# Kernel optimization log

Hardware: AMD Instinct MI355X
Metric: run time of the kernel (lower is better)

Reference implementation:

```python
import jax, jax.numpy as jnp
import numpy as np

G = 4      # deformable groups
K = 9      # 3x3 kernel points
EPS = 1e-5


def _bilinear_gather(value, loc_y, loc_x):
    # value: (N,H,W,G,Cg); loc_*: (N,H,W,G,K) float pixel coords, zero padding outside.
    N, H, W, g, Cg = value.shape
    y0f = jnp.floor(loc_y); x0f = jnp.floor(loc_x)
    wy = loc_y - y0f; wx = loc_x - x0f
    y0 = y0f.astype(jnp.int32); x0 = x0f.astype(jnp.int32)
    n_idx = jnp.arange(N).reshape(N, 1, 1, 1, 1)
    g_idx = jnp.arange(g).reshape(1, 1, 1, g, 1)

    def corner(yi, xi, w):
        valid = (yi >= 0) & (yi < H) & (xi >= 0) & (xi < W)
        yc = jnp.clip(yi, 0, H - 1); xc = jnp.clip(xi, 0, W - 1)
        v = value[n_idx, yc, xc, g_idx]  # (N,H,W,G,K,Cg) irregular gather
        return v * (w * valid)[..., None]

    return (corner(y0, x0, (1 - wy) * (1 - wx))
            + corner(y0, x0 + 1, (1 - wy) * wx)
            + corner(y0 + 1, x0, wy * (1 - wx))
            + corner(y0 + 1, x0 + 1, wy * wx))


def _dcnv4(t, H, W, Wv, bv, Wom, bom, Wo):
    # DCNv4 on (N,L,C): value proj -> learned-offset bilinear sampling with
    # UNNORMALIZED dynamic weights (no softmax, DCNv4) -> output proj (no bias).
    N, L, C = t.shape
    Cg = C // G
    value = (t @ Wv + bv).reshape(N, H, W, G, Cg)
    om = (t @ Wom + bom).reshape(N, H, W, G, 3 * K)
    offset = om[..., :2 * K].reshape(N, H, W, G, K, 2)  # (dx, dy) per point
    mask = om[..., 2 * K:]                               # (N,H,W,G,K)
    ky, kx = jnp.meshgrid(jnp.arange(-1, 2), jnp.arange(-1, 2), indexing='ij')
    ky = ky.reshape(-1).astype(t.dtype); kx = kx.reshape(-1).astype(t.dtype)
    ys = jnp.arange(H, dtype=t.dtype).reshape(1, H, 1, 1, 1)
    xs = jnp.arange(W, dtype=t.dtype).reshape(1, 1, W, 1, 1)
    loc_y = ys + ky + offset[..., 1]  # (N,H,W,G,K)
    loc_x = xs + kx + offset[..., 0]
    sampled = _bilinear_gather(value, loc_y, loc_x)  # (N,H,W,G,K,Cg)
    out = (sampled * mask[..., None]).sum(axis=4)    # (N,H,W,G,Cg)
    return out.reshape(N, L, C) @ Wo


def _bn(x, gamma, beta):
    # training-mode BatchNorm2d: per-channel batch stats over (N,H,W)
    mean = x.mean(axis=(0, 2, 3), keepdims=True)
    var = ((x - mean) ** 2).mean(axis=(0, 2, 3), keepdims=True)
    return (x - mean) * jax.lax.rsqrt(var + EPS) * gamma.reshape(1, -1, 1, 1) \
        + beta.reshape(1, -1, 1, 1)


def setup_inputs() -> dict:
    key = jax.random.key(0)
    ks = jax.random.split(key, 6)
    N, C, H, W = 4, 128, 64, 64
    s = 1.0 / np.sqrt(C)
    x = jax.random.normal(ks[0], (N, C, H, W), jnp.float32)
    Wv = jax.random.normal(ks[1], (C, C), jnp.float32) * s      # value_proj
    bv = jnp.zeros((C,), jnp.float32)
    Wom = jax.random.normal(ks[2], (C, G * 3 * K), jnp.float32) * 0.01  # offset+mask head
    bom = jnp.zeros((G * 3 * K,), jnp.float32)
    Wo = jax.random.normal(ks[3], (C, C), jnp.float32) * s      # output_proj (bias=False)
    gamma = jnp.ones((C,), jnp.float32)
    beta = jnp.zeros((C,), jnp.float32)
    Wc = jax.random.normal(ks[4], (C, C), jnp.float32) * s      # 1x1 conv (out=in=C)
    return {"x": x, "Wv": Wv, "bv": bv, "Wom": Wom, "bom": bom,
            "Wo": Wo, "gamma": gamma, "beta": beta, "Wc": Wc}


def reference(x, Wv, bv, Wom, bom, Wo, gamma, beta, Wc):
    N, C, H, W = x.shape
    shortcut = x
    t = x.transpose(0, 2, 3, 1).reshape(N, H * W, C)
    t = _dcnv4(t, H, W, Wv, bv, Wom, bom, Wo)
    y = t.reshape(N, H, W, C).transpose(0, 3, 1, 2)
    y = jax.nn.relu(_bn(y, gamma, beta))
    t = y.transpose(0, 2, 3, 1).reshape(N, H * W, C)
    t = _dcnv4(t, H, W, Wv, bv, Wom, bom, Wo)  # same DCNv4 weights reused
    y = t.reshape(N, H, W, C).transpose(0, 3, 1, 2)
    y = _bn(y, gamma, beta)                    # same BN params reused, no relu here
    y = y + shortcut                           # in_channels == out_channels
    return jnp.einsum('nchw,oc->nohw', y, Wc)  # final 1x1 conv
```

## Files before the change

### kernel.cpp

```cpp
#include <hip/hip_runtime.h>
#include <math.h>

#define CC   128
#define NL   16384
#define LHW  4096
#define OMP  112
#define HH   64
#define WW   64

typedef __attribute__((ext_vector_type(8))) short short8;
typedef __attribute__((ext_vector_type(4))) float f32x4;

__device__ __forceinline__ unsigned short f2bf(float f) {
    union { float f; unsigned u; } v; v.f = f;
    unsigned r = v.u + 0x7fff + ((v.u >> 16) & 1);
    return (unsigned short)(r >> 16);
}
__device__ __forceinline__ float bf2f(unsigned short u) {
    union { unsigned u; float f; } v; v.u = ((unsigned)u) << 16;
    return v.f;
}

__global__ __launch_bounds__(256) void prep_kernel(
    const float* __restrict__ Wv, const float* __restrict__ Wom,
    const float* __restrict__ Wo, const float* __restrict__ Wc,
    unsigned short* __restrict__ Wcomb, unsigned short* __restrict__ WoT,
    unsigned short* __restrict__ Wcb, float* __restrict__ stats)
{
    int tid = threadIdx.x;
    if (blockIdx.x == 0) {
        stats[tid] = 0.0f;
        stats[256 + tid] = 0.0f;
    }
    int i = blockIdx.x * 256 + tid;
    if (i < 16384) {
        int n = i >> 7, k = i & 127;
        Wcomb[i] = f2bf(Wv[k * CC + n]);
    } else if (i < 30720) {
        int j = i - 16384; int n = j >> 7, k = j & 127;
        Wcomb[16384 + j] = (n < 108) ? f2bf(Wom[k * 108 + n]) : (unsigned short)0;
    } else if (i < 47104) {
        int j = i - 30720; int n = j >> 7, k = j & 127;
        WoT[j] = f2bf(Wo[k * CC + n]);
    } else if (i < 63488) {
        int j = i - 47104;
        Wcb[j] = f2bf(Wc[j]);
    }
}

template<int IN_MODE>
__global__ __launch_bounds__(256) void gemm_vom_kernel(
    const float* __restrict__ Ain, const unsigned short* __restrict__ Wcomb,
    const float* __restrict__ bv, const float* __restrict__ bom,
    const float* __restrict__ stats, const float* __restrict__ gamma,
    const float* __restrict__ beta,
    unsigned short* __restrict__ val, float* __restrict__ omb)
{
    __shared__ unsigned short As[64 * 136];
    __shared__ unsigned short Bs[240 * 136];
    __shared__ float bnsc[128], bnsh[128];

    int tid = threadIdx.x;
    int block_m = blockIdx.x * 64;

    if (IN_MODE == 1 && tid < 128) {
        const float inv = 1.0f / 16384.0f;
        float mean = stats[tid] * inv;
        float var  = stats[128 + tid] * inv - mean * mean;
        float sc   = rsqrtf(var + 1e-5f) * gamma[tid];
        bnsc[tid] = sc;
        bnsh[tid] = beta[tid] - mean * sc;
    }

#pragma unroll
    for (int i = 0; i < 15; i++) {
        int id = tid + i * 256;
        int r = id >> 4, kc = id & 15;
        float4 v = *(const float4*)(Wcomb + (size_t)r * CC + kc * 8);
        *(float4*)(&Bs[r * 136 + kc * 8]) = v;
    }

    if (IN_MODE == 0) {
        int n   = block_m >> 12;
        int hw0 = block_m & 4095;
#pragma unroll
        for (int i = 0; i < 8; i++) {
            int id = tid + i * 256;
            int c  = id >> 4, j4 = id & 15;
            float4 v = *(const float4*)(Ain + (((size_t)(n * CC + c)) << 12) + hw0 + j4 * 4);
            As[(j4 * 4 + 0) * 136 + c] = f2bf(v.x);
            As[(j4 * 4 + 1) * 136 + c] = f2bf(v.y);
            As[(j4 * 4 + 2) * 136 + c] = f2bf(v.z);
            As[(j4 * 4 + 3) * 136 + c] = f2bf(v.w);
        }
    } else {
        __syncthreads();
#pragma unroll
        for (int i = 0; i < 8; i++) {
            int id = tid + i * 256;
            int r  = id >> 5, c4 = id & 31;
            float4 v = *(const float4*)(Ain + (size_t)(block_m + r) * CC + c4 * 4);
            int c = c4 * 4;
            float a0 = fmaxf(v.x * bnsc[c + 0] + bnsh[c + 0], 0.0f);
            float a1 = fmaxf(v.y * bnsc[c + 1] + bnsh[c + 1], 0.0f);
            float a2 = fmaxf(v.z * bnsc[c + 2] + bnsh[c + 2], 0.0f);
            float a3 = fmaxf(v.w * bnsc[c + 3] + bnsh[c + 3], 0.0f);
            As[r * 136 + c + 0] = f2bf(a0);
            As[r * 136 + c + 1] = f2bf(a1);
            As[r * 136 + c + 2] = f2bf(a2);
            As[r * 136 + c + 3] = f2bf(a3);
        }
    }
    __syncthreads();

    int w  = tid >> 6;
    int l  = tid & 63;
    int lr = l & 15, lk = l >> 4;

    f32x4 acc[15];
#pragma unroll
    for (int nt = 0; nt < 15; nt++) acc[nt] = (f32x4){0.f, 0.f, 0.f, 0.f};

#pragma unroll
    for (int kk = 0; kk < 4; kk++) {
        short8 a = *(const short8*)(&As[(w * 16 + lr) * 136 + kk * 32 + lk * 8]);
#pragma unroll
        for (int nt = 0; nt < 15; nt++) {
            short8 b = *(const short8*)(&Bs[(nt * 16 + lr) * 136 + kk * 32 + lk * 8]);
            acc[nt] = __builtin_amdgcn_mfma_f32_16x16x32_bf16(a, b, acc[nt], 0, 0, 0);
        }
    }

    int row0 = block_m + w * 16 + lk * 4;
#pragma unroll
    for (int nt = 0; nt < 8; nt++) {
        int col = nt * 16 + lr;
        float bb = bv[col];
#pragma unroll
        for (int r = 0; r < 4; r++)
            val[(size_t)(row0 + r) * CC + col] = f2bf(acc[nt][r] + bb);
    }
#pragma unroll
    for (int nt = 8; nt < 15; nt++) {
        int col = (nt - 8) * 16 + lr;
        float bb = (col < 108) ? bom[col] : 0.0f;
#pragma unroll
        for (int r = 0; r < 4; r++)
            omb[(size_t)(row0 + r) * OMP + col] = acc[nt][r] + bb;
    }
}

__global__ __launch_bounds__(256) void sample_kernel(
    const unsigned short* __restrict__ val, const float* __restrict__ omb,
    unsigned int* __restrict__ sbuf)
{
    int tid    = threadIdx.x;
    int gid    = blockIdx.x * 256 + tid;
    int unit   = gid >> 4;
    int lane16 = gid & 15;
    int nl = unit >> 2;
    int g  = unit & 3;
    int n  = nl >> 12;
    int hw = nl & 4095;
    int h  = hw >> 6;
    int w  = hw & 63;

    const float* omp = omb + (size_t)nl * OMP + g * 27;
    const unsigned short* vb = val + (((size_t)n) << 19) + g * 32 + lane16 * 2;

    float acc0 = 0.0f, acc1 = 0.0f;
#pragma unroll
    for (int k = 0; k < 9; k++) {
        float ox = omp[2 * k];
        float oy = omp[2 * k + 1];
        float mk = omp[18 + k];
        float ly = (float)(h + k / 3 - 1) + oy;
        float lx = (float)(w + k % 3 - 1) + ox;
        float y0f = floorf(ly), x0f = floorf(lx);
        float wy = ly - y0f, wx = lx - x0f;
        int y0 = (int)y0f, x0 = (int)x0f;

        float v0 = 0.0f, v1 = 0.0f;
#pragma unroll
        for (int cy = 0; cy < 2; cy++) {
#pragma unroll
            for (int cx = 0; cx < 2; cx++) {
                int yi = y0 + cy, xi = x0 + cx;
                float wgt = (cy ? wy : 1.0f - wy) * (cx ? wx : 1.0f - wx);
                bool valid = (yi >= 0) && (yi < HH) && (xi >= 0) && (xi < WW);
                wgt = valid ? wgt : 0.0f;
                int yc = min(max(yi, 0), HH - 1);
                int xc = min(max(xi, 0), WW - 1);
                unsigned int pv = *(const unsigned int*)(vb + (size_t)(yc * WW + xc) * CC);
                v0 += bf2f((unsigned short)(pv & 0xffff)) * wgt;
                v1 += bf2f((unsigned short)(pv >> 16)) * wgt;
            }
        }
        acc0 += mk * v0;
        acc1 += mk * v1;
    }
    unsigned int packed = (unsigned int)f2bf(acc0) | ((unsigned int)f2bf(acc1) << 16);
    sbuf[(size_t)nl * 64 + g * 16 + lane16] = packed;
}

__global__ __launch_bounds__(256) void gemm_o_bn_kernel(
    const unsigned short* __restrict__ A, const unsigned short* __restrict__ Bt,
    float* __restrict__ ybuf, float* __restrict__ stats)
{
    __shared__ unsigned short As[64 * 136];
    __shared__ unsigned short Bs[128 * 136];
    __shared__ float lstat[256];

    int tid = threadIdx.x;
    int block_m = blockIdx.x * 64;
    lstat[tid] = 0.0f;

#pragma unroll
    for (int i = 0; i < 4; i++) {
        int id = tid + i * 256;
        int r = id >> 4, kc = id & 15;
        float4 v = *(const float4*)(A + (size_t)(block_m + r) * CC + kc * 8);
        *(float4*)(&As[r * 136 + kc * 8]) = v;
    }
#pragma unroll
    for (int i = 0; i < 8; i++) {
        int id = tid + i * 256;
        int r = id >> 4, kc = id & 15;
        float4 v = *(const float4*)(Bt + (size_t)r * CC + kc * 8);
        *(float4*)(&Bs[r * 136 + kc * 8]) = v;
    }
    __syncthreads();

    int w  = tid >> 6;
    int l  = tid & 63;
    int wm = w & 1, wn = w >> 1;
    int lr = l & 15, lk = l >> 4;

    f32x4 acc[2][4];
#pragma unroll
    for (int mt = 0; mt < 2; mt++)
#pragma unroll
        for (int nt = 0; nt < 4; nt++) acc[mt][nt] = (f32x4){0.f, 0.f, 0.f, 0.f};

#pragma unroll
    for (int kk = 0; kk < 4; kk++) {
        short8 a[2], b[4];
#pragma unroll
        for (int mt = 0; mt < 2; mt++)
            a[mt] = *(const short8*)(&As[(wm * 32 + mt * 16 + lr) * 136 + kk * 32 + lk * 8]);
#pragma unroll
        for (int nt = 0; nt < 4; nt++)
            b[nt] = *(const short8*)(&Bs[(wn * 64 + nt * 16 + lr) * 136 + kk * 32 + lk * 8]);
#pragma unroll
        for (int mt = 0; mt < 2; mt++)
#pragma unroll
            for (int nt = 0; nt < 4; nt++)
                acc[mt][nt] = __builtin_amdgcn_mfma_f32_16x16x32_bf16(
                    a[mt], b[nt], acc[mt][nt], 0, 0, 0);
    }

#pragma unroll
    for (int nt = 0; nt < 4; nt++) {
        int col = wn * 64 + nt * 16 + lr;
        float s = 0.0f, sq = 0.0f;
#pragma unroll
        for (int mt = 0; mt < 2; mt++) {
            int row0 = block_m + wm * 32 + mt * 16 + lk * 4;
#pragma unroll
            for (int r = 0; r < 4; r++) {
                float v = acc[mt][nt][r];
                ybuf[(size_t)(row0 + r) * CC + col] = v;
                s += v;
                sq += v * v;
            }
        }
        atomicAdd(&lstat[col], s);
        atomicAdd(&lstat[128 + col], sq);
    }
    __syncthreads();
    if (tid < 128) {
        atomicAdd(&stats[tid], lstat[tid]);
        atomicAdd(&stats[128 + tid], lstat[128 + tid]);
    }
}

__global__ __launch_bounds__(256) void gemm_final_kernel(
    const float* __restrict__ ybuf, const float* __restrict__ x,
    const unsigned short* __restrict__ Bt, const float* __restrict__ stats,
    const float* __restrict__ gamma, const float* __restrict__ beta,
    float* __restrict__ out)
{
    __shared__ unsigned short As[64 * 136];
    __shared__ unsigned short Bs[128 * 136];
    __shared__ float Xs[64 * 132];
    __shared__ float bnsc[128], bnsh[128];

    int tid = threadIdx.x;
    int block_m = blockIdx.x * 64;
    int n   = block_m >> 12;
    int hw0 = block_m & 4095;

    if (tid < 128) {
        const float inv = 1.0f / 16384.0f;
        float mean = stats[tid] * inv;
        float var  = stats[128 + tid] * inv - mean * mean;
        float sc   = rsqrtf(var + 1e-5f) * gamma[tid];
        bnsc[tid] = sc;
        bnsh[tid] = beta[tid] - mean * sc;
    }

#pragma unroll
    for (int i = 0; i < 8; i++) {
        int id = tid + i * 256;
        int c  = id >> 4, j4 = id & 15;
        float4 v = *(const float4*)(x + (((size_t)(n * CC + c)) << 12) + hw0 + j4 * 4);
        Xs[(j4 * 4 + 0) * 132 + c] = v.x;
        Xs[(j4 * 4 + 1) * 132 + c] = v.y;
        Xs[(j4 * 4 + 2) * 132 + c] = v.z;
        Xs[(j4 * 4 + 3) * 132 + c] = v.w;
    }
#pragma unroll
    for (int i = 0; i < 8; i++) {
        int id = tid + i * 256;
        int r = id >> 4, kc = id & 15;
        float4 v = *(const float4*)(Bt + (size_t)r * CC + kc * 8);
        *(float4*)(&Bs[r * 136 + kc * 8]) = v;
    }
    __syncthreads();

#pragma unroll
    for (int i = 0; i < 8; i++) {
        int id = tid + i * 256;
        int r  = id >> 5, c4 = id & 31;
        float4 v = *(const float4*)(ybuf + (size_t)(block_m + r) * CC + c4 * 4);
        int c = c4 * 4;
        float a0 = v.x * bnsc[c + 0] + bnsh[c + 0] + Xs[r * 132 + c + 0];
        float a1 = v.y * bnsc[c + 1] + bnsh[c + 1] + Xs[r * 132 + c + 1];
        float a2 = v.z * bnsc[c + 2] + bnsh[c + 2] + Xs[r * 132 + c + 2];
        float a3 = v.w * bnsc[c + 3] + bnsh[c + 3] + Xs[r * 132 + c + 3];
        As[r * 136 + c + 0] = f2bf(a0);
        As[r * 136 + c + 1] = f2bf(a1);
        As[r * 136 + c + 2] = f2bf(a2);
        As[r * 136 + c + 3] = f2bf(a3);
    }
    __syncthreads();

    int w  = tid >> 6;
    int l  = tid & 63;
    int wm = w & 1, wn = w >> 1;
    int lr = l & 15, lk = l >> 4;

    f32x4 acc[2][4];
#pragma unroll
    for (int mt = 0; mt < 2; mt++)
#pragma unroll
        for (int nt = 0; nt < 4; nt++) acc[mt][nt] = (f32x4){0.f, 0.f, 0.f, 0.f};

#pragma unroll
    for (int kk = 0; kk < 4; kk++) {
        short8 a[2], b[4];
#pragma unroll
        for (int mt = 0; mt < 2; mt++)
            a[mt] = *(const short8*)(&As[(wm * 32 + mt * 16 + lr) * 136 + kk * 32 + lk * 8]);
#pragma unroll
        for (int nt = 0; nt < 4; nt++)
            b[nt] = *(const short8*)(&Bs[(wn * 64 + nt * 16 + lr) * 136 + kk * 32 + lk * 8]);
#pragma unroll
        for (int mt = 0; mt < 2; mt++)
#pragma unroll
            for (int nt = 0; nt < 4; nt++)
                acc[mt][nt] = __builtin_amdgcn_mfma_f32_16x16x32_bf16(
                    a[mt], b[nt], acc[mt][nt], 0, 0, 0);
    }

    __syncthreads();
    float* T = (float*)Bs;
#pragma unroll
    for (int mt = 0; mt < 2; mt++) {
        int rloc = wm * 32 + mt * 16 + lk * 4;
#pragma unroll
        for (int nt = 0; nt < 4; nt++) {
            int col = wn * 64 + nt * 16 + lr;
#pragma unroll
            for (int r = 0; r < 4; r++)
                T[col * 68 + rloc + r] = acc[mt][nt][r];
        }
    }
    __syncthreads();
    int o = tid >> 1, half = tid & 1;
    float* op = out + (((size_t)(n * CC + o)) << 12) + hw0 + half * 32;
#pragma unroll
    for (int i = 0; i < 8; i++) {
        float4 v = *(const float4*)(&T[o * 68 + half * 32 + i * 4]);
        *(float4*)(op + i * 4) = v;
    }
}

extern "C" void kernel_launch(void* const* d_in, const int* in_sizes, int n_in,
                              void* d_out, int out_size, void* d_ws, size_t ws_size,
                              hipStream_t stream)
{
    const float* x     = (const float*)d_in[0];
    const float* Wv    = (const float*)d_in[1];
    const float* bv    = (const float*)d_in[2];
    const float* Wom   = (const float*)d_in[3];
    const float* bom   = (const float*)d_in[4];
    const float* Wo    = (const float*)d_in[5];
    const float* gamma = (const float*)d_in[6];
    const float* beta  = (const float*)d_in[7];
    const float* Wc    = (const float*)d_in[8];
    float* out = (float*)d_out;

    char* ws = (char*)d_ws;
    unsigned short* val   = (unsigned short*)ws;   ws += (size_t)NL * CC * 2;
    float*          omb   = (float*)ws;            ws += (size_t)NL * OMP * 4;
    unsigned int*   sbuf  = (unsigned int*)ws;     ws += (size_t)NL * CC * 2;
    float*          ybuf  = (float*)ws;            ws += (size_t)NL * CC * 4;
    unsigned short* Wcomb = (unsigned short*)ws;   ws += 240 * 128 * 2;
    unsigned short* WoT   = (unsigned short*)ws;   ws += 128 * 128 * 2;
    unsigned short* Wcb   = (unsigned short*)ws;   ws += 128 * 128 * 2;
    float*          stats = (float*)ws;            ws += 2048;

    dim3 b256(256);

    prep_kernel<<<248, b256, 0, stream>>>(Wv, Wom, Wo, Wc, Wcomb, WoT, Wcb, stats);

    gemm_vom_kernel<0><<<256, b256, 0, stream>>>(x, Wcomb, bv, bom,
                                                 nullptr, nullptr, nullptr, val, omb);
    sample_kernel<<<4096, b256, 0, stream>>>(val, omb, sbuf);
    gemm_o_bn_kernel<<<256, b256, 0, stream>>>((const unsigned short*)sbuf, WoT, ybuf, stats);

    gemm_vom_kernel<1><<<256, b256, 0, stream>>>(ybuf, Wcomb, bv, bom,
                                                 stats, gamma, beta, val, omb);
    sample_kernel<<<4096, b256, 0, stream>>>(val, omb, sbuf);
    gemm_o_bn_kernel<<<256, b256, 0, stream>>>((const unsigned short*)sbuf, WoT, ybuf, stats + 256);

    gemm_final_kernel<<<256, b256, 0, stream>>>(ybuf, x, Wcb, stats + 256, gamma, beta, out);
}
```

Baseline: 157.5 us.

## Shrink GEMM tiles to 16 rows, read weights from global, shard BN stats atomics

All GEMM kernels now process 16-row tiles with 1024 blocks instead of 64-row tiles with 256 blocks. The B weight tiles are no longer staged in shared memory; MFMA operands are loaded straight from global memory, which relies on L2/L1 caching of the small bf16 weight matrices. BN statistics are accumulated into 8 sharded slots that consumers sum, to reduce atomic contention on one address set. The aim is higher occupancy and better CU coverage on the small GEMMs, at the cost of redundant global weight reads and uncoalesced fragment loads.

```diff
diff --git a/kernel.cpp b/kernel.cpp
--- a/kernel.cpp
+++ b/kernel.cpp
@@ -3,7 +3,6 @@
 
 #define CC   128
 #define NL   16384
-#define LHW  4096
 #define OMP  112
 #define HH   64
 #define WW   64
@@ -28,22 +27,21 @@
     unsigned short* __restrict__ Wcb, float* __restrict__ stats)
 {
     int tid = threadIdx.x;
-    if (blockIdx.x == 0) {
-        stats[tid] = 0.0f;
-        stats[256 + tid] = 0.0f;
-    }
-    int i = blockIdx.x * 256 + tid;
-    if (i < 16384) {
-        int n = i >> 7, k = i & 127;
-        Wcomb[i] = f2bf(Wv[k * CC + n]);
-    } else if (i < 30720) {
-        int j = i - 16384; int n = j >> 7, k = j & 127;
-        Wcomb[16384 + j] = (n < 108) ? f2bf(Wom[k * 108 + n]) : (unsigned short)0;
-    } else if (i < 47104) {
-        int j = i - 30720; int n = j >> 7, k = j & 127;
-        WoT[j] = f2bf(Wo[k * CC + n]);
-    } else if (i < 63488) {
-        int j = i - 47104;
+    int b   = blockIdx.x;
+    if (b < 16) stats[b * 256 + tid] = 0.0f;
+    int i = b * 256 + tid;
+    if (i < 32768) {
+        int r = i >> 7, k = i & 127;
+        unsigned short v;
+        if (r < 128)      v = f2bf(Wv[k * CC + r]);
+        else if (r < 240) { int nn = r - 128; v = (nn < 108) ? f2bf(Wom[k * 108 + nn]) : (unsigned short)0; }
+        else              v = 0;
+        Wcomb[i] = v;
+    } else if (i < 49152) {
+        int j = i - 32768; int nn = j >> 7, k = j & 127;
+        WoT[j] = f2bf(Wo[k * CC + nn]);
+    } else {
+        int j = i - 49152;
         Wcb[j] = f2bf(Wc[j]);
     }
 }
@@ -56,37 +54,37 @@
     const float* __restrict__ beta,
     unsigned short* __restrict__ val, float* __restrict__ omb)
 {
-    __shared__ unsigned short As[64 * 136];
-    __shared__ unsigned short Bs[240 * 136];
+    __shared__ unsigned short As[16 * 136];
     __shared__ float bnsc[128], bnsh[128];
 
     int tid = threadIdx.x;
-    int block_m = blockIdx.x * 64;
-
-    if (IN_MODE == 1 && tid < 128) {
-        const float inv = 1.0f / 16384.0f;
-        float mean = stats[tid] * inv;
-        float var  = stats[128 + tid] * inv - mean * mean;
-        float sc   = rsqrtf(var + 1e-5f) * gamma[tid];
-        bnsc[tid] = sc;
-        bnsh[tid] = beta[tid] - mean * sc;
-    }
-
-#pragma unroll
-    for (int i = 0; i < 15; i++) {
-        int id = tid + i * 256;
-        int r = id >> 4, kc = id & 15;
-        float4 v = *(const float4*)(Wcomb + (size_t)r * CC + kc * 8);
-        *(float4*)(&Bs[r * 136 + kc * 8]) = v;
+    int block_m = blockIdx.x * 16;
+
+    if (IN_MODE == 1) {
+        if (tid < 128) {
+            float s = 0.0f, sq = 0.0f;
+#pragma unroll
+            for (int g = 0; g < 8; g++) {
+                s  += stats[g * 256 + tid];
+                sq += stats[g * 256 + 128 + tid];
+            }
+            const float inv = 1.0f / 16384.0f;
+            float mean = s * inv;
+            float var  = sq * inv - mean * mean;
+            float sc   = rsqrtf(var + 1e-5f) * gamma[tid];
+            bnsc[tid] = sc;
+            bnsh[tid] = beta[tid] - mean * sc;
+        }
+        __syncthreads();
     }
 
     if (IN_MODE == 0) {
         int n   = block_m >> 12;
         int hw0 = block_m & 4095;
 #pragma unroll
-        for (int i = 0; i < 8; i++) {
+        for (int i = 0; i < 2; i++) {
             int id = tid + i * 256;
-            int c  = id >> 4, j4 = id & 15;
+            int c  = id >> 2, j4 = id & 3;
             float4 v = *(const float4*)(Ain + (((size_t)(n * CC + c)) << 12) + hw0 + j4 * 4);
             As[(j4 * 4 + 0) * 136 + c] = f2bf(v.x);
             As[(j4 * 4 + 1) * 136 + c] = f2bf(v.y);
@@ -94,21 +92,15 @@
             As[(j4 * 4 + 3) * 136 + c] = f2bf(v.w);
         }
     } else {
-        __syncthreads();
-#pragma unroll
-        for (int i = 0; i < 8; i++) {
+#pragma unroll
+        for (int i = 0; i < 2; i++) {
             int id = tid + i * 256;
-            int r  = id >> 5, c4 = id & 31;
-            float4 v = *(const float4*)(Ain + (size_t)(block_m + r) * CC + c4 * 4);
-            int c = c4 * 4;
-            float a0 = fmaxf(v.x * bnsc[c + 0] + bnsh[c + 0], 0.0f);
-            float a1 = fmaxf(v.y * bnsc[c + 1] + bnsh[c + 1], 0.0f);
-            float a2 = fmaxf(v.z * bnsc[c + 2] + bnsh[c + 2], 0.0f);
-            float a3 = fmaxf(v.w * bnsc[c + 3] + bnsh[c + 3], 0.0f);
-            As[r * 136 + c + 0] = f2bf(a0);
-            As[r * 136 + c + 1] = f2bf(a1);
-            As[r * 136 + c + 2] = f2bf(a2);
-            As[r * 136 + c + 3] = f2bf(a3);
+            int r  = id >> 5, c = (id & 31) * 4;
+            float4 v = *(const float4*)(Ain + (size_t)(block_m + r) * CC + c);
+            As[r * 136 + c + 0] = f2bf(fmaxf(v.x * bnsc[c + 0] + bnsh[c + 0], 0.0f));
+            As[r * 136 + c + 1] = f2bf(fmaxf(v.y * bnsc[c + 1] + bnsh[c + 1], 0.0f));
+            As[r * 136 + c + 2] = f2bf(fmaxf(v.z * bnsc[c + 2] + bnsh[c + 2], 0.0f));
+            As[r * 136 + c + 3] = f2bf(fmaxf(v.w * bnsc[c + 3] + bnsh[c + 3], 0.0f));
         }
     }
     __syncthreads();
@@ -117,36 +109,37 @@
     int l  = tid & 63;
     int lr = l & 15, lk = l >> 4;
 
-    f32x4 acc[15];
-#pragma unroll
-    for (int nt = 0; nt < 15; nt++) acc[nt] = (f32x4){0.f, 0.f, 0.f, 0.f};
+    f32x4 acc[4];
+#pragma unroll
+    for (int nt = 0; nt < 4; nt++) acc[nt] = (f32x4){0.f, 0.f, 0.f, 0.f};
 
 #pragma unroll
     for (int kk = 0; kk < 4; kk++) {
-        short8 a = *(const short8*)(&As[(w * 16 + lr) * 136 + kk * 32 + lk * 8]);
-#pragma unroll
-        for (int nt = 0; nt < 15; nt++) {
-            short8 b = *(const short8*)(&Bs[(nt * 16 + lr) * 136 + kk * 32 + lk * 8]);
+        short8 a = *(const short8*)(&As[lr * 136 + kk * 32 + lk * 8]);
+#pragma unroll
+        for (int nt = 0; nt < 4; nt++) {
+            int ntile = w + nt * 4;
+            short8 b = *(const short8*)(Wcomb + (size_t)(ntile * 16 + lr) * CC + kk * 32 + lk * 8);
             acc[nt] = __builtin_amdgcn_mfma_f32_16x16x32_bf16(a, b, acc[nt], 0, 0, 0);
         }
     }
 
-    int row0 = block_m + w * 16 + lk * 4;
-#pragma unroll
-    for (int nt = 0; nt < 8; nt++) {
-        int col = nt * 16 + lr;
-        float bb = bv[col];
-#pragma unroll
-        for (int r = 0; r < 4; r++)
-            val[(size_t)(row0 + r) * CC + col] = f2bf(acc[nt][r] + bb);
-    }
-#pragma unroll
-    for (int nt = 8; nt < 15; nt++) {
-        int col = (nt - 8) * 16 + lr;
-        float bb = (col < 108) ? bom[col] : 0.0f;
-#pragma unroll
-        for (int r = 0; r < 4; r++)
-            omb[(size_t)(row0 + r) * OMP + col] = acc[nt][r] + bb;
+    int row0 = block_m + lk * 4;
+#pragma unroll
+    for (int nt = 0; nt < 4; nt++) {
+        int col = (w + nt * 4) * 16 + lr;
+        if (col < 128) {
+            float bb = bv[col];
+#pragma unroll
+            for (int r = 0; r < 4; r++)
+                val[(size_t)(row0 + r) * CC + col] = f2bf(acc[nt][r] + bb);
+        } else if (col < 240) {
+            int oc = col - 128;
+            float bb = (oc < 108) ? bom[oc] : 0.0f;
+#pragma unroll
+            for (int r = 0; r < 4; r++)
+                omb[(size_t)(row0 + r) * OMP + oc] = acc[nt][r] + bb;
+        }
     }
 }
 
@@ -207,80 +200,50 @@
     const unsigned short* __restrict__ A, const unsigned short* __restrict__ Bt,
     float* __restrict__ ybuf, float* __restrict__ stats)
 {
-    __shared__ unsigned short As[64 * 136];
-    __shared__ unsigned short Bs[128 * 136];
     __shared__ float lstat[256];
-
     int tid = threadIdx.x;
-    int block_m = blockIdx.x * 64;
+    int block_m = blockIdx.x * 16;
     lstat[tid] = 0.0f;
-
-#pragma unroll
-    for (int i = 0; i < 4; i++) {
-        int id = tid + i * 256;
-        int r = id >> 4, kc = id & 15;
-        float4 v = *(const float4*)(A + (size_t)(block_m + r) * CC + kc * 8);
-        *(float4*)(&As[r * 136 + kc * 8]) = v;
-    }
-#pragma unroll
-    for (int i = 0; i < 8; i++) {
-        int id = tid + i * 256;
-        int r = id >> 4, kc = id & 15;
-        float4 v = *(const float4*)(Bt + (size_t)r * CC + kc * 8);
-        *(float4*)(&Bs[r * 136 + kc * 8]) = v;
-    }
     __syncthreads();
 
     int w  = tid >> 6;
     int l  = tid & 63;
-    int wm = w & 1, wn = w >> 1;
     int lr = l & 15, lk = l >> 4;
 
-    f32x4 acc[2][4];
-#pragma unroll
-    for (int mt = 0; mt < 2; mt++)
-#pragma unroll
-        for (int nt = 0; nt < 4; nt++) acc[mt][nt] = (f32x4){0.f, 0.f, 0.f, 0.f};
+    f32x4 acc[2];
+    acc[0] = (f32x4){0.f, 0.f, 0.f, 0.f};
+    acc[1] = (f32x4){0.f, 0.f, 0.f, 0.f};
 
 #pragma unroll
     for (int kk = 0; kk < 4; kk++) {
-        short8 a[2], b[4];
-#pragma unroll
-        for (int mt = 0; mt < 2; mt++)
-            a[mt] = *(const short8*)(&As[(wm * 32 + mt * 16 + lr) * 136 + kk * 32 + lk * 8]);
-#pragma unroll
-        for (int nt = 0; nt < 4; nt++)
-            b[nt] = *(const short8*)(&Bs[(wn * 64 + nt * 16 + lr) * 136 + kk * 32 + lk * 8]);
-#pragma unroll
-        for (int mt = 0; mt < 2; mt++)
-#pragma unroll
-            for (int nt = 0; nt < 4; nt++)
-                acc[mt][nt] = __builtin_amdgcn_mfma_f32_16x16x32_bf16(
-                    a[mt], b[nt], acc[mt][nt], 0, 0, 0);
-    }
-
-#pragma unroll
-    for (int nt = 0; nt < 4; nt++) {
-        int col = wn * 64 + nt * 16 + lr;
+        short8 a = *(const short8*)(A + (size_t)(block_m + lr) * CC + kk * 32 + lk * 8);
+#pragma unroll
+        for (int nt = 0; nt < 2; nt++) {
+            short8 b = *(const short8*)(Bt + (size_t)((w * 2 + nt) * 16 + lr) * CC + kk * 32 + lk * 8);
+            acc[nt] = __builtin_amdgcn_mfma_f32_16x16x32_bf16(a, b, acc[nt], 0, 0, 0);
+        }
+    }
+
+    int row0 = block_m + lk * 4;
+#pragma unroll
+    for (int nt = 0; nt < 2; nt++) {
+        int col = (w * 2 + nt) * 16 + lr;
         float s = 0.0f, sq = 0.0f;
 #pragma unroll
-        for (int mt = 0; mt < 2; mt++) {
-            int row0 = block_m + wm * 32 + mt * 16 + lk * 4;
-#pragma unroll
-            for (int r = 0; r < 4; r++) {
-                float v = acc[mt][nt][r];
-                ybuf[(size_t)(row0 + r) * CC + col] = v;
-                s += v;
-                sq += v * v;
-            }
+        for (int r = 0; r < 4; r++) {
+            float v = acc[nt][r];
+            ybuf[(size_t)(row0 + r) * CC + col] = v;
+            s += v;
+            sq += v * v;
         }
         atomicAdd(&lstat[col], s);
         atomicAdd(&lstat[128 + col], sq);
     }
     __syncthreads();
     if (tid < 128) {
-        atomicAdd(&stats[tid], lstat[tid]);
-        atomicAdd(&stats[128 + tid], lstat[128 + tid]);
+        float* sg = stats + (blockIdx.x & 7) * 256;
+        atomicAdd(&sg[tid], lstat[tid]);
+        atomicAdd(&sg[128 + tid], lstat[128 + tid]);
     }
 }
 
@@ -290,109 +253,87 @@
     const float* __restrict__ gamma, const float* __restrict__ beta,
     float* __restrict__ out)
 {
-    __shared__ unsigned short As[64 * 136];
-    __shared__ unsigned short Bs[128 * 136];
-    __shared__ float Xs[64 * 132];
+    __shared__ unsigned short As[16 * 136];
+    __shared__ float Xs[16 * 132];
+    __shared__ float T[128 * 20];
     __shared__ float bnsc[128], bnsh[128];
 
     int tid = threadIdx.x;
-    int block_m = blockIdx.x * 64;
+    int block_m = blockIdx.x * 16;
     int n   = block_m >> 12;
     int hw0 = block_m & 4095;
 
     if (tid < 128) {
+        float s = 0.0f, sq = 0.0f;
+#pragma unroll
+        for (int g = 0; g < 8; g++) {
+            s  += stats[g * 256 + tid];
+            sq += stats[g * 256 + 128 + tid];
+        }
         const float inv = 1.0f / 16384.0f;
-        float mean = stats[tid] * inv;
-        float var  = stats[128 + tid] * inv - mean * mean;
+        float mean = s * inv;
+        float var  = sq * inv - mean * mean;
         float sc   = rsqrtf(var + 1e-5f) * gamma[tid];
         bnsc[tid] = sc;
         bnsh[tid] = beta[tid] - mean * sc;
     }
 
 #pragma unroll
-    for (int i = 0; i < 8; i++) {
+    for (int i = 0; i < 2; i++) {
         int id = tid + i * 256;
-        int c  = id >> 4, j4 = id & 15;
+        int c  = id >> 2, j4 = id & 3;
         float4 v = *(const float4*)(x + (((size_t)(n * CC + c)) << 12) + hw0 + j4 * 4);
         Xs[(j4 * 4 + 0) * 132 + c] = v.x;
         Xs[(j4 * 4 + 1) * 132 + c] = v.y;
         Xs[(j4 * 4 + 2) * 132 + c] = v.z;
         Xs[(j4 * 4 + 3) * 132 + c] = v.w;
     }
-#pragma unroll
-    for (int i = 0; i < 8; i++) {
+    __syncthreads();
+
+#pragma unroll
+    for (int i = 0; i < 2; i++) {
         int id = tid + i * 256;
-        int r = id >> 4, kc = id & 15;
-        float4 v = *(const float4*)(Bt + (size_t)r * CC + kc * 8);
-        *(float4*)(&Bs[r * 136 + kc * 8]) = v;
-    }
-    __syncthreads();
-
-#pragma unroll
-    for (int i = 0; i < 8; i++) {
-        int id = tid + i * 256;
-        int r  = id >> 5, c4 = id & 31;
-        float4 v = *(const float4*)(ybuf + (size_t)(block_m + r) * CC + c4 * 4);
-        int c = c4 * 4;
-        float a0 = v.x * bnsc[c + 0] + bnsh[c + 0] + Xs[r * 132 + c + 0];
-        float a1 = v.y * bnsc[c + 1] + bnsh[c + 1] + Xs[r * 132 + c + 1];
-        float a2 = v.z * bnsc[c + 2] + bnsh[c + 2] + Xs[r * 132 + c + 2];
-        float a3 = v.w * bnsc[c + 3] + bnsh[c + 3] + Xs[r * 132 + c + 3];
-        As[r * 136 + c + 0] = f2bf(a0);
-        As[r * 136 + c + 1] = f2bf(a1);
-        As[r * 136 + c + 2] = f2bf(a2);
-        As[r * 136 + c + 3] = f2bf(a3);
+        int r  = id >> 5, c = (id & 31) * 4;
+        float4 v = *(const float4*)(ybuf + (size_t)(block_m + r) * CC + c);
+        As[r * 136 + c + 0] = f2bf(v.x * bnsc[c + 0] + bnsh[c + 0] + Xs[r * 132 + c + 0]);
+        As[r * 136 + c + 1] = f2bf(v.y * bnsc[c + 1] + bnsh[c + 1] + Xs[r * 132 + c + 1]);
+        As[r * 136 + c + 2] = f2bf(v.z * bnsc[c + 2] + bnsh[c + 2] + Xs[r * 132 + c + 2]);
+        As[r * 136 + c + 3] = f2bf(v.w * bnsc[c + 3] + bnsh[c + 3] + Xs[r * 132 + c + 3]);
     }
     __syncthreads();
 
     int w  = tid >> 6;
     int l  = tid & 63;
-    int wm = w & 1, wn = w >> 1;
     int lr = l & 15, lk = l >> 4;
 
-    f32x4 acc[2][4];
-#pragma unroll
-    for (int mt = 0; mt < 2; mt++)
-#pragma unroll
-        for (int nt = 0; nt < 4; nt++) acc[mt][nt] = (f32x4){0.f, 0.f, 0.f, 0.f};
+    f32x4 acc[2];
+    acc[0] = (f32x4){0.f, 0.f, 0.f, 0.f};
+    acc[1] = (f32x4){0.f, 0.f, 0.f, 0.f};
 
 #pragma unroll
     for (int kk = 0; kk < 4; kk++) {
-        short8 a[2], b[4];
-#pragma unroll
-        for (int mt = 0; mt < 2; mt++)
-            a[mt] = *(const short8*)(&As[(wm * 32 + mt * 16 + lr) * 136 + kk * 32 + lk * 8]);
-#pragma unroll
-        for (int nt = 0; nt < 4; nt++)
-            b[nt] = *(const short8*)(&Bs[(wn * 64 + nt * 16 + lr) * 136 + kk * 32 + lk * 8]);
-#pragma unroll
-        for (int mt = 0; mt < 2; mt++)
-#pragma unroll
-            for (int nt = 0; nt < 4; nt++)
-                acc[mt][nt] = __builtin_amdgcn_mfma_f32_16x16x32_bf16(
-                    a[mt], b[nt], acc[mt][nt], 0, 0, 0);
-    }
-
-    __syncthreads();
-    float* T = (float*)Bs;
-#pragma unroll
-    for (int mt = 0; mt < 2; mt++) {
-        int rloc = wm * 32 + mt * 16 + lk * 4;
-#pragma unroll
-        for (int nt = 0; nt < 4; nt++) {
-            int col = wn * 64 + nt * 16 + lr;
-#pragma unroll
-            for (int r = 0; r < 4; r++)
-                T[col * 68 + rloc + r] = acc[mt][nt][r];
-        }
-    }
-    __syncthreads();
-    int o = tid >> 1, half = tid & 1;
-    float* op = out + (((size_t)(n * CC + o)) << 12) + hw0 + half * 32;
-#pragma unroll
-    for (int i = 0; i < 8; i++) {
-        float4 v = *(const float4*)(&T[o * 68 + half * 32 + i * 4]);
-        *(float4*)(op + i * 4) = v;
+        short8 a = *(const short8*)(&As[lr * 136 + kk * 32 + lk * 8]);
+#pragma unroll
+        for (int nt = 0; nt < 2; nt++) {
+            short8 b = *(const short8*)(Bt + (size_t)((w * 2 + nt) * 16 + lr) * CC + kk * 32 + lk * 8);
+            acc[nt] = __builtin_amdgcn_mfma_f32_16x16x32_bf16(a, b, acc[nt], 0, 0, 0);
+        }
+    }
+
+#pragma unroll
+    for (int nt = 0; nt < 2; nt++) {
+        int col = (w * 2 + nt) * 16 + lr;
+#pragma unroll
+        for (int r = 0; r < 4; r++)
+            T[col * 20 + lk * 4 + r] = acc[nt][r];
+    }
+    __syncthreads();
+#pragma unroll
+    for (int i = 0; i < 2; i++) {
+        int id = tid + i * 256;
+        int o  = id >> 2, j4 = id & 3;
+        float4 v = *(const float4*)(&T[o * 20 + j4 * 4]);
+        *(float4*)(out + (((size_t)(n * CC + o)) << 12) + hw0 + j4 * 4) = v;
     }
 }
 
@@ -416,24 +357,24 @@
     float*          omb   = (float*)ws;            ws += (size_t)NL * OMP * 4;
     unsigned int*   sbuf  = (unsigned int*)ws;     ws += (size_t)NL * CC * 2;
     float*          ybuf  = (float*)ws;            ws += (size_t)NL * CC * 4;
-    unsigned short* Wcomb = (unsigned short*)ws;   ws += 240 * 128 * 2;
+    unsigned short* Wcomb = (unsigned short*)ws;   ws += 256 * 128 * 2;
     unsigned short* WoT   = (unsigned short*)ws;   ws += 128 * 128 * 2;
     unsigned short* Wcb   = (unsigned short*)ws;   ws += 128 * 128 * 2;
-    float*          stats = (float*)ws;            ws += 2048;
+    float*          stats = (float*)ws;            ws += 4096 * 4;
 
     dim3 b256(256);
 
-    prep_kernel<<<248, b256, 0, stream>>>(Wv, Wom, Wo, Wc, Wcomb, WoT, Wcb, stats);
-
-    gemm_vom_kernel<0><<<256, b256, 0, stream>>>(x, Wcomb, bv, bom,
-                                                 nullptr, nullptr, nullptr, val, omb);
+    prep_kernel<<<256, b256, 0, stream>>>(Wv, Wom, Wo, Wc, Wcomb, WoT, Wcb, stats);
+
+    gemm_vom_kernel<0><<<1024, b256, 0, stream>>>(x, Wcomb, bv, bom,
+                                                  nullptr, nullptr, nullptr, val, omb);
     sample_kernel<<<4096, b256, 0, stream>>>(val, omb, sbuf);
-    gemm_o_bn_kernel<<<256, b256, 0, stream>>>((const unsigned short*)sbuf, WoT, ybuf, stats);
-
-    gemm_vom_kernel<1><<<256, b256, 0, stream>>>(ybuf, Wcomb, bv, bom,
-                                                 stats, gamma, beta, val, omb);
+    gemm_o_bn_kernel<<<1024, b256, 0, stream>>>((const unsigned short*)sbuf, WoT, ybuf, stats);
+
+    gemm_vom_kernel<1><<<1024, b256, 0, stream>>>(ybuf, Wcomb, bv, bom,
+                                                  stats, gamma, beta, val, omb);
     sample_kernel<<<4096, b256, 0, stream>>>(val, omb, sbuf);
-    gemm_o_bn_kernel<<<256, b256, 0, stream>>>((const unsigned short*)sbuf, WoT, ybuf, stats + 256);
-
-    gemm_final_kernel<<<256, b256, 0, stream>>>(ybuf, x, Wcb, stats + 256, gamma, beta, out);
-}
+    gemm_o_bn_kernel<<<1024, b256, 0, stream>>>((const unsigned short*)sbuf, WoT, ybuf, stats + 2048);
+
+    gemm_final_kernel<<<1024, b256, 0, stream>>>(ybuf, x, Wcb, stats + 2048, gamma, beta, out);
+}
```

Result: slower. 167.9 us (+6.6%).
